# Optimization experiments

Measured on AMD Instinct MI355X. Metric: run time of the kernel, lower is better.

Reference implementation:

```python
import jax, jax.numpy as jnp
import numpy as np

N_NODES = 50000
N_EDGES = 800000
D_IN = 64
D_OUT = 64
D_HID = 64
EPS = 1e-5


def _init_params(key):
    ks = jax.random.split(key, 12)
    s = 0.05
    p = {}
    p["W_lin"] = jax.random.normal(ks[0], (D_IN, D_OUT), jnp.float32) * s
    p["W_src"] = jax.random.normal(ks[1], (D_IN, D_OUT), jnp.float32) * s
    p["W_dst"] = jax.random.normal(ks[2], (D_IN, D_OUT), jnp.float32) * s
    p["pos_w1"] = jax.random.normal(ks[3], (3, D_HID), jnp.float32) * s
    p["pos_b1"] = jnp.zeros((D_HID,), jnp.float32)
    p["pos_w2"] = jax.random.normal(ks[4], (D_HID, D_OUT), jnp.float32) * s
    p["pos_b2"] = jnp.zeros((D_OUT,), jnp.float32)
    p["attn_w1"] = jax.random.normal(ks[5], (D_OUT, D_HID), jnp.float32) * s
    p["attn_b1"] = jnp.zeros((D_HID,), jnp.float32)
    p["attn_w2"] = jax.random.normal(ks[6], (D_HID, D_OUT), jnp.float32) * s
    p["attn_b2"] = jnp.zeros((D_OUT,), jnp.float32)
    p["gamma"] = jnp.ones((D_OUT,), jnp.float32)
    p["beta"] = jnp.zeros((D_OUT,), jnp.float32)
    return p


def setup_inputs() -> dict:
    key = jax.random.key(0)
    k1, k2, k3, k4 = jax.random.split(key, 4)
    inp = {
        "x": jax.random.normal(k1, (N_NODES, D_IN), jnp.float32),
        "pos": jax.random.normal(k2, (N_NODES, 3), jnp.float32),
        "edge_index": jax.random.randint(k3, (2, N_EDGES), 0, N_NODES, jnp.int64),
    }
    inp.update(_init_params(k4))
    return inp


def _segment_softmax(alpha, seg, num_segments):
    # channel-wise softmax over edges sharing the same destination node
    m = jax.ops.segment_max(alpha, seg, num_segments=num_segments)  # [N, D]
    e = jnp.exp(alpha - m[seg])
    z = jax.ops.segment_sum(e, seg, num_segments=num_segments)  # [N, D]
    return e / (z[seg] + 1e-16)


def reference(x, pos, edge_index, W_lin, W_src, W_dst,
              pos_w1, pos_b1, pos_w2, pos_b2,
              attn_w1, attn_b1, attn_w2, attn_b2, gamma, beta):
    N = x.shape[0]
    # add self loops (PointTransformerConv default add_self_loops=True)
    loops = jnp.arange(N, dtype=edge_index.dtype)
    src = jnp.concatenate([edge_index[0], loops])  # j
    dst = jnp.concatenate([edge_index[1], loops])  # i (aggregation target)

    x_val = x @ W_lin          # [N, D] value projection
    a_src = x @ W_src          # alpha_j source term
    a_dst = x @ W_dst          # alpha_i destination term

    # per-edge positional encoding: pos_nn(pos_i - pos_j), two Linears, no activation
    rel = pos[dst] - pos[src]                         # [E, 3]
    delta = (rel @ pos_w1 + pos_b1) @ pos_w2 + pos_b2  # [E, D]

    # attention logits: attn_nn(alpha_i - alpha_j + delta)
    alpha = a_dst[dst] - a_src[src] + delta
    alpha = (alpha @ attn_w1 + attn_b1) @ attn_w2 + attn_b2  # [E, D]
    alpha = _segment_softmax(alpha, dst, N)

    # message and scatter-sum aggregation
    msg = alpha * (x_val[src] + delta)                # [E, D]
    out = jax.ops.segment_sum(msg, dst, num_segments=N)  # [N, D]

    out = jax.nn.elu(out)

    # BatchNorm over nodes (training-mode batch stats, biased var, eps=1e-5)
    mean = jnp.mean(out, axis=0)
    var = jnp.var(out, axis=0)
    out = (out - mean) * jax.lax.rsqrt(var + EPS) * gamma + beta
    return out
```

## Files before the change

kernel.cpp:

```cpp
#include <hip/hip_runtime.h>
#include <cmath>


__device__ __forceinline__ unsigned bf16r(float f) {
    unsigned u = __float_as_uint(f);
    return (u + 0x7fffu + ((u >> 16) & 1u)) >> 16;
}
__device__ __forceinline__ float bfhi(unsigned u) { return __uint_as_float(u & 0xffff0000u); }
__device__ __forceinline__ float bflo(unsigned u) { return __uint_as_float(u << 16); }

__device__ __forceinline__ void gemm_tile(const float (*xs)[68], const float (*Wl)[64],
                                          int tx, int ty, float acc[4][4])
{
    #pragma unroll
    for (int i = 0; i < 4; ++i)
        #pragma unroll
        for (int j = 0; j < 4; ++j) acc[i][j] = 0.f;
    for (int k = 0; k < 64; k += 4) {
        float4 b0 = *(const float4*)&Wl[k + 0][4 * tx];
        float4 b1 = *(const float4*)&Wl[k + 1][4 * tx];
        float4 b2 = *(const float4*)&Wl[k + 2][4 * tx];
        float4 b3 = *(const float4*)&Wl[k + 3][4 * tx];
        #pragma unroll
        for (int i = 0; i < 4; ++i) {
            float4 a = *(const float4*)&xs[4 * ty + i][k];
            acc[i][0] += a.x * b0.x + a.y * b1.x + a.z * b2.x + a.w * b3.x;
            acc[i][1] += a.x * b0.y + a.y * b1.y + a.z * b2.y + a.w * b3.y;
            acc[i][2] += a.x * b0.z + a.y * b1.z + a.z * b2.z + a.w * b3.z;
            acc[i][3] += a.x * b0.w + a.y * b1.w + a.z * b2.w + a.w * b3.w;
        }
    }
}

__global__ __launch_bounds__(256) void k_pre1(
    const float* __restrict__ attn_w1, const float* __restrict__ attn_w2,
    const float* __restrict__ pos_w1, const float* __restrict__ pos_b1,
    const float* __restrict__ pos_w2, const float* __restrict__ pos_b2,
    float* __restrict__ A2, float* __restrict__ M3, float* __restrict__ bc)
{
    int t = threadIdx.x;
    if (blockIdx.x == 0) {
        __shared__ __align__(16) float As[64][68];
        __shared__ __align__(16) float Bs[64][64];
        int lk = t & 63, lr = t >> 6;
        for (int i = 0; i < 16; ++i) {
            As[lr + 4 * i][lk] = attn_w1[(lr + 4 * i) * 64 + lk];
            Bs[lr + 4 * i][lk] = attn_w2[(lr + 4 * i) * 64 + lk];
        }
        __syncthreads();
        int tx = t & 15, ty = t >> 4;
        float acc[4][4];
        gemm_tile(As, Bs, tx, ty, acc);
        #pragma unroll
        for (int i = 0; i < 4; ++i)
            *(float4*)&A2[(4 * ty + i) * 64 + 4 * tx] =
                make_float4(acc[i][0], acc[i][1], acc[i][2], acc[i][3]);
    } else {
        int c = t & 63, q = t >> 6;
        if (q < 3) {
            float acc = 0.f;
            for (int h = 0; h < 64; ++h) acc += pos_w1[q * 64 + h] * pos_w2[h * 64 + c];
            M3[q * 64 + c] = acc;
        } else {
            float accb = 0.f;
            for (int h = 0; h < 64; ++h) accb += pos_b1[h] * pos_w2[h * 64 + c];
            bc[c] = accb + pos_b2[c];
        }
    }
}

__global__ __launch_bounds__(256) void k_pre2(
    const float* __restrict__ W_src, const float* __restrict__ A2,
    const float* __restrict__ M3,
    float* __restrict__ Wsrc2, float* __restrict__ M5)
{
    int t = threadIdx.x;
    if (blockIdx.x == 0) {
        __shared__ __align__(16) float As[64][68];
        __shared__ __align__(16) float Bs[64][64];
        int lk = t & 63, lr = t >> 6;
        for (int i = 0; i < 16; ++i) {
            As[lr + 4 * i][lk] = W_src[(lr + 4 * i) * 64 + lk];
            Bs[lr + 4 * i][lk] = A2[(lr + 4 * i) * 64 + lk];
        }
        __syncthreads();
        int tx = t & 15, ty = t >> 4;
        float acc[4][4];
        gemm_tile(As, Bs, tx, ty, acc);
        #pragma unroll
        for (int i = 0; i < 4; ++i)
            *(float4*)&Wsrc2[(4 * ty + i) * 64 + 4 * tx] =
                make_float4(acc[i][0], acc[i][1], acc[i][2], acc[i][3]);
    } else {
        int c = t & 63, q = t >> 6;
        if (q < 3) {
            float acc = 0.f;
            for (int k = 0; k < 64; ++k) acc += M3[q * 64 + k] * A2[k * 64 + c];
            M5[q * 64 + c] = acc;
        }
    }
}

__global__ __launch_bounds__(256, 4) void k_gemm_pair(
    const float* __restrict__ x, const float* __restrict__ pos,
    const float* __restrict__ Wsrc2, const float* __restrict__ Wlin,
    const float* __restrict__ M3, const float* __restrict__ M5,
    unsigned* __restrict__ pairbf, int n_nodes)
{
    __shared__ __align__(16) float xs[64][68];
    __shared__ __align__(16) float Wl[64][64];
    __shared__ float ps[192];
    __shared__ float m3s[192], m5s[192];
    int t = threadIdx.x;
    int tx = t & 15;
    int ty = t >> 4;
    int nbase = blockIdx.x * 64;
    int lk = t & 63;
    int lr = t >> 6;

    for (int i = 0; i < 16; ++i) {
        int n = lr + 4 * i;
        int gn = nbase + n;
        xs[n][lk] = (gn < n_nodes) ? x[gn * 64 + lk] : 0.f;
    }
    if (t < 192) {
        int gi = nbase * 3 + t;
        ps[t] = (gi < n_nodes * 3) ? pos[gi] : 0.f;
        m3s[t] = M3[t];
        m5s[t] = M5[t];
    }
    for (int i = 0; i < 16; ++i) Wl[lr + 4 * i][lk] = Wsrc2[(lr + 4 * i) * 64 + lk];
    __syncthreads();

    float acc_s[4][4];
    gemm_tile(xs, Wl, tx, ty, acc_s);

    __syncthreads();
    for (int i = 0; i < 16; ++i) Wl[lr + 4 * i][lk] = Wlin[(lr + 4 * i) * 64 + lk];
    __syncthreads();

    float acc_x[4][4];
    gemm_tile(xs, Wl, tx, ty, acc_x);

    #pragma unroll
    for (int i = 0; i < 4; ++i) {
        int n = 4 * ty + i;
        int gn = nbase + n;
        if (gn < n_nodes) {
            float px = ps[3 * n], py = ps[3 * n + 1], pz = ps[3 * n + 2];
            int c0 = 4 * tx;
            float g50 = px * m5s[c0]     + py * m5s[64 + c0]     + pz * m5s[128 + c0];
            float g51 = px * m5s[c0 + 1] + py * m5s[64 + c0 + 1] + pz * m5s[128 + c0 + 1];
            float g52 = px * m5s[c0 + 2] + py * m5s[64 + c0 + 2] + pz * m5s[128 + c0 + 2];
            float g53 = px * m5s[c0 + 3] + py * m5s[64 + c0 + 3] + pz * m5s[128 + c0 + 3];
            float g30 = px * m3s[c0]     + py * m3s[64 + c0]     + pz * m3s[128 + c0];
            float g31 = px * m3s[c0 + 1] + py * m3s[64 + c0 + 1] + pz * m3s[128 + c0 + 1];
            float g32 = px * m3s[c0 + 2] + py * m3s[64 + c0 + 2] + pz * m3s[128 + c0 + 2];
            float g33 = px * m3s[c0 + 3] + py * m3s[64 + c0 + 3] + pz * m3s[128 + c0 + 3];
            uint4 w;
            w.x = (bf16r(__expf(-(acc_s[i][0] + g50))) << 16) | bf16r(acc_x[i][0] - g30);
            w.y = (bf16r(__expf(-(acc_s[i][1] + g51))) << 16) | bf16r(acc_x[i][1] - g31);
            w.z = (bf16r(__expf(-(acc_s[i][2] + g52))) << 16) | bf16r(acc_x[i][2] - g32);
            w.w = (bf16r(__expf(-(acc_s[i][3] + g53))) << 16) | bf16r(acc_x[i][3] - g33);
            *(uint4*)&pairbf[gn * 64 + c0] = w;
        }
    }
}

__global__ __launch_bounds__(256) void k_hist(const int* __restrict__ ei,
                                              int* __restrict__ cnt, int n_edges)
{
    int i = blockIdx.x * blockDim.x + threadIdx.x;
    if (i < n_edges) atomicAdd(&cnt[ei[n_edges + i]], 1);
}

#define SCAN_CHUNK 4096

__global__ __launch_bounds__(256) void k_scan_partial(const int* __restrict__ cnt,
                                                      int* __restrict__ bsum, int n)
{
    __shared__ int wsh[4];
    int b = blockIdx.x, t = threadIdx.x;
    int base = b * SCAN_CHUNK + t * 16;
    int s = 0;
    #pragma unroll
    for (int i = 0; i < 16; ++i) {
        int idx = base + i;
        if (idx < n) s += cnt[idx];
    }
    for (int off = 32; off; off >>= 1) s += __shfl_down(s, off, 64);
    int lane = t & 63, wv = t >> 6;
    if (lane == 0) wsh[wv] = s;
    __syncthreads();
    if (t == 0) bsum[b] = wsh[0] + wsh[1] + wsh[2] + wsh[3];
}

__global__ void k_scan_base(const int* __restrict__ bsum, int* __restrict__ bbase,
                            int* __restrict__ rowptr, int nch, int n, int n_edges)
{
    if (threadIdx.x == 0) {
        int acc = 0;
        for (int c = 0; c < nch; ++c) { int tmp = bsum[c]; bbase[c] = acc; acc += tmp; }
        rowptr[n] = n_edges;
    }
}

__global__ __launch_bounds__(256) void k_scan_final(const int* __restrict__ cnt,
                                                    const int* __restrict__ bbase,
                                                    int* __restrict__ rowptr,
                                                    int* __restrict__ cursor, int n)
{
    __shared__ int wsh[4];
    int b = blockIdx.x, t = threadIdx.x;
    int base = b * SCAN_CHUNK + t * 16;
    int v[16];
    int s = 0;
    #pragma unroll
    for (int i = 0; i < 16; ++i) {
        int idx = base + i;
        v[i] = (idx < n) ? cnt[idx] : 0;
        s += v[i];
    }
    int lane = t & 63, wv = t >> 6;
    int inc = s;
    for (int off = 1; off < 64; off <<= 1) {
        int u = __shfl_up(inc, off, 64);
        if (lane >= off) inc += u;
    }
    if (lane == 63) wsh[wv] = inc;
    __syncthreads();
    if (t == 0) {
        int acc = 0;
        for (int w = 0; w < 4; ++w) { int tmp = wsh[w]; wsh[w] = acc; acc += tmp; }
    }
    __syncthreads();
    int run = bbase[b] + wsh[wv] + inc - s;
    #pragma unroll
    for (int i = 0; i < 16; ++i) {
        int idx = base + i;
        if (idx < n) {
            rowptr[idx] = run;
            cursor[idx] = run;
            run += v[i];
        }
    }
}

__global__ __launch_bounds__(256) void k_scatter(const int* __restrict__ ei,
                                                 int* __restrict__ cursor,
                                                 int* __restrict__ csr_src,
                                                 int n_edges)
{
    int i = blockIdx.x * blockDim.x + threadIdx.x;
    if (i < n_edges) {
        int dst = ei[n_edges + i];
        int p = atomicAdd(&cursor[dst], 1);
        csr_src[p] = ei[i] * 64;
    }
}

__global__ __launch_bounds__(256) void k_gather(
    const int* __restrict__ rowptr, const int* __restrict__ csr_src,
    const unsigned* __restrict__ pairbf, const float* __restrict__ pos,
    const float* __restrict__ M3, const float* __restrict__ bc,
    float* __restrict__ out, float* __restrict__ stats, int n_nodes)
{
    int t = threadIdx.x;
    int c = t & 63;
    float bcc = bc[c];
    float m30 = M3[c], m31 = M3[64 + c], m32 = M3[128 + c];

    int wid = (blockIdx.x * blockDim.x + t) >> 6;
    int nw = (gridDim.x * blockDim.x) >> 6;

    float lsum = 0.f, lsq = 0.f;

    for (int i = wid; i < n_nodes; i += nw) {
        int beg = rowptr[i], end = rowptr[i + 1];
        float px = pos[3 * i], py = pos[3 * i + 1], pz = pos[3 * i + 2];
        float ddi = bcc + px * m30 + py * m31 + pz * m32;
        unsigned up = pairbf[i * 64 + c];
        float w = bfhi(up);
        float zz = w;
        float SS = w * (bflo(up) + ddi);

        int k = beg;
        for (; k + 8 <= end; k += 8) {
            int s0 = csr_src[k],     s1 = csr_src[k + 1];
            int s2 = csr_src[k + 2], s3 = csr_src[k + 3];
            int s4 = csr_src[k + 4], s5 = csr_src[k + 5];
            int s6 = csr_src[k + 6], s7 = csr_src[k + 7];
            unsigned u0 = pairbf[s0 + c], u1 = pairbf[s1 + c];
            unsigned u2 = pairbf[s2 + c], u3 = pairbf[s3 + c];
            unsigned u4 = pairbf[s4 + c], u5 = pairbf[s5 + c];
            unsigned u6 = pairbf[s6 + c], u7 = pairbf[s7 + c];
            float w0 = bfhi(u0), w1 = bfhi(u1), w2 = bfhi(u2), w3 = bfhi(u3);
            float w4 = bfhi(u4), w5 = bfhi(u5), w6 = bfhi(u6), w7 = bfhi(u7);
            zz += ((w0 + w1) + (w2 + w3)) + ((w4 + w5) + (w6 + w7));
            SS += w0 * (bflo(u0) + ddi) + w1 * (bflo(u1) + ddi)
                + w2 * (bflo(u2) + ddi) + w3 * (bflo(u3) + ddi)
                + w4 * (bflo(u4) + ddi) + w5 * (bflo(u5) + ddi)
                + w6 * (bflo(u6) + ddi) + w7 * (bflo(u7) + ddi);
        }
        for (; k < end; ++k) {
            unsigned u0 = pairbf[csr_src[k] + c];
            float w0 = bfhi(u0);
            zz += w0;
            SS += w0 * (bflo(u0) + ddi);
        }

        float v = SS / (zz + 1e-16f);
        v = (v > 0.f) ? v : expm1f(v);
        out[i * 64 + c] = v;
        lsum += v;
        lsq += v * v;
    }

    __shared__ float sred[256], sred2[256];
    sred[t] = lsum;
    sred2[t] = lsq;
    __syncthreads();
    if (t < 64) {
        float s = sred[t] + sred[t + 64] + sred[t + 128] + sred[t + 192];
        float q = sred2[t] + sred2[t + 64] + sred2[t + 128] + sred2[t + 192];
        unsafeAtomicAdd(&stats[t], s);
        unsafeAtomicAdd(&stats[64 + t], q);
    }
}

__global__ __launch_bounds__(256) void k_bn(
    float4* __restrict__ out4, const float* __restrict__ stats,
    const float* __restrict__ gamma, const float* __restrict__ beta,
    int total4, float inv_n)
{
    __shared__ float ssc[64], ssh[64];
    int t = threadIdx.x;
    if (t < 64) {
        float mean = stats[t] * inv_n;
        float var = stats[64 + t] * inv_n - mean * mean;
        float scale = (1.0f / sqrtf(var + 1e-5f)) * gamma[t];
        ssc[t] = scale;
        ssh[t] = beta[t] - mean * scale;
    }
    __syncthreads();
    for (int idx = blockIdx.x * blockDim.x + t; idx < total4;
         idx += gridDim.x * blockDim.x) {
        float4 v = out4[idx];
        int c0 = (idx << 2) & 63;
        v.x = v.x * ssc[c0]     + ssh[c0];
        v.y = v.y * ssc[c0 + 1] + ssh[c0 + 1];
        v.z = v.z * ssc[c0 + 2] + ssh[c0 + 2];
        v.w = v.w * ssc[c0 + 3] + ssh[c0 + 3];
        out4[idx] = v;
    }
}

extern "C" void kernel_launch(void* const* d_in, const int* in_sizes, int n_in,
                              void* d_out, int out_size, void* d_ws, size_t ws_size,
                              hipStream_t stream)
{
    const float* x        = (const float*)d_in[0];
    const float* pos      = (const float*)d_in[1];
    const int*   ei       = (const int*)d_in[2];
    const float* W_lin    = (const float*)d_in[3];
    const float* W_src    = (const float*)d_in[4];
    const float* pos_w1   = (const float*)d_in[6];
    const float* pos_b1   = (const float*)d_in[7];
    const float* pos_w2   = (const float*)d_in[8];
    const float* pos_b2   = (const float*)d_in[9];
    const float* attn_w1  = (const float*)d_in[10];
    const float* attn_w2  = (const float*)d_in[12];
    const float* gamma    = (const float*)d_in[14];
    const float* beta     = (const float*)d_in[15];

    int n_nodes = in_sizes[0] / 64;
    int n_edges = in_sizes[2] / 2;
    int total = n_nodes * 64;
    int nch = (n_nodes + SCAN_CHUNK - 1) / SCAN_CHUNK;

    unsigned* pairbf = (unsigned*)d_ws;
    float* A2    = (float*)(pairbf + total);
    float* Wsrc2 = A2 + 4096;
    float* M3    = Wsrc2 + 4096;
    float* M5    = M3 + 192;
    float* bc    = M5 + 192;
    float* stats = bc + 64;
    int*   cnt     = (int*)(stats + 128);
    int*   rowptr  = cnt + n_nodes;
    int*   cursor  = rowptr + n_nodes + 1;
    int*   csr_src = cursor + n_nodes;
    int*   bsum    = csr_src + n_edges;
    int*   bbase   = bsum + 64;

    hipMemsetAsync(cnt, 0, (size_t)n_nodes * sizeof(int), stream);
    hipMemsetAsync(stats, 0, 128 * sizeof(float), stream);

    k_pre1<<<2, 256, 0, stream>>>(attn_w1, attn_w2, pos_w1, pos_b1, pos_w2,
                                  pos_b2, A2, M3, bc);
    k_pre2<<<2, 256, 0, stream>>>(W_src, A2, M3, Wsrc2, M5);
    k_gemm_pair<<<(n_nodes + 63) / 64, 256, 0, stream>>>(
        x, pos, Wsrc2, W_lin, M3, M5, pairbf, n_nodes);
    k_hist<<<(n_edges + 255) / 256, 256, 0, stream>>>(ei, cnt, n_edges);
    k_scan_partial<<<nch, 256, 0, stream>>>(cnt, bsum, n_nodes);
    k_scan_base<<<1, 64, 0, stream>>>(bsum, bbase, rowptr, nch, n_nodes, n_edges);
    k_scan_final<<<nch, 256, 0, stream>>>(cnt, bbase, rowptr, cursor, n_nodes);
    k_scatter<<<(n_edges + 255) / 256, 256, 0, stream>>>(ei, cursor, csr_src, n_edges);
    k_gather<<<2048, 256, 0, stream>>>(rowptr, csr_src, pairbf, pos, M3, bc,
                                       (float*)d_out, stats, n_nodes);
    k_bn<<<2048, 256, 0, stream>>>((float4*)d_out, stats, gamma, beta, total / 4,
                                   1.0f / (float)n_nodes);
}
```

Before: 223.0 us.

## Fuse memsets, histogram and scan-base into neighbouring kernels to cut launches

Zeroing of the count and stats buffers moves into extra blocks of the first precompute kernel, replacing two memsets. The edge histogram runs in extra blocks appended to the node GEMM kernel, so the two overlap inside one launch. The separate single-thread scan-base kernel is folded into the final scan, where each block sums the preceding block totals itself. The gather loop also factors the per-node positional term out of the weighted sum and adds it after normalisation, saving an add per edge but dropping the 1e-16 guard on the denominator.

```diff
diff --git a/kernel.cpp b/kernel.cpp
--- a/kernel.cpp
+++ b/kernel.cpp
@@ -36,7 +36,8 @@
     const float* __restrict__ attn_w1, const float* __restrict__ attn_w2,
     const float* __restrict__ pos_w1, const float* __restrict__ pos_b1,
     const float* __restrict__ pos_w2, const float* __restrict__ pos_b2,
-    float* __restrict__ A2, float* __restrict__ M3, float* __restrict__ bc)
+    float* __restrict__ A2, float* __restrict__ M3, float* __restrict__ bc,
+    int* __restrict__ cnt, float* __restrict__ stats, int n_nodes)
 {
     int t = threadIdx.x;
     if (blockIdx.x == 0) {
@@ -55,7 +56,7 @@
         for (int i = 0; i < 4; ++i)
             *(float4*)&A2[(4 * ty + i) * 64 + 4 * tx] =
                 make_float4(acc[i][0], acc[i][1], acc[i][2], acc[i][3]);
-    } else {
+    } else if (blockIdx.x == 1) {
         int c = t & 63, q = t >> 6;
         if (q < 3) {
             float acc = 0.f;
@@ -66,6 +67,11 @@
             for (int h = 0; h < 64; ++h) accb += pos_b1[h] * pos_w2[h * 64 + c];
             bc[c] = accb + pos_b2[c];
         }
+    } else {
+        if (blockIdx.x == 2 && t < 128) stats[t] = 0.f;
+        int idx = (blockIdx.x - 2) * 256 + t;
+        int stride = (gridDim.x - 2) * 256;
+        for (int i = idx; i < n_nodes; i += stride) cnt[i] = 0;
     }
 }
 
@@ -101,17 +107,25 @@
     }
 }
 
-__global__ __launch_bounds__(256, 4) void k_gemm_pair(
+__global__ __launch_bounds__(256, 4) void k_gemm_pair_hist(
     const float* __restrict__ x, const float* __restrict__ pos,
     const float* __restrict__ Wsrc2, const float* __restrict__ Wlin,
     const float* __restrict__ M3, const float* __restrict__ M5,
-    unsigned* __restrict__ pairbf, int n_nodes)
-{
+    unsigned* __restrict__ pairbf, int n_nodes,
+    const int* __restrict__ ei, int* __restrict__ cnt, int n_edges, int G)
+{
+    int t = threadIdx.x;
+    if ((int)blockIdx.x >= G) {
+        int idx = ((int)blockIdx.x - G) * 256 + t;
+        int stride = ((int)gridDim.x - G) * 256;
+        for (int i = idx; i < n_edges; i += stride)
+            atomicAdd(&cnt[ei[n_edges + i]], 1);
+        return;
+    }
     __shared__ __align__(16) float xs[64][68];
     __shared__ __align__(16) float Wl[64][64];
     __shared__ float ps[192];
     __shared__ float m3s[192], m5s[192];
-    int t = threadIdx.x;
     int tx = t & 15;
     int ty = t >> 4;
     int nbase = blockIdx.x * 64;
@@ -167,13 +181,6 @@
     }
 }
 
-__global__ __launch_bounds__(256) void k_hist(const int* __restrict__ ei,
-                                              int* __restrict__ cnt, int n_edges)
-{
-    int i = blockIdx.x * blockDim.x + threadIdx.x;
-    if (i < n_edges) atomicAdd(&cnt[ei[n_edges + i]], 1);
-}
-
 #define SCAN_CHUNK 4096
 
 __global__ __launch_bounds__(256) void k_scan_partial(const int* __restrict__ cnt,
@@ -195,23 +202,21 @@
     if (t == 0) bsum[b] = wsh[0] + wsh[1] + wsh[2] + wsh[3];
 }
 
-__global__ void k_scan_base(const int* __restrict__ bsum, int* __restrict__ bbase,
-                            int* __restrict__ rowptr, int nch, int n, int n_edges)
-{
-    if (threadIdx.x == 0) {
+__global__ __launch_bounds__(256) void k_scan_final(const int* __restrict__ cnt,
+                                                    const int* __restrict__ bsum,
+                                                    int* __restrict__ rowptr,
+                                                    int* __restrict__ cursor,
+                                                    int n, int nch, int n_edges)
+{
+    __shared__ int wsh[4];
+    __shared__ int bb;
+    int b = blockIdx.x, t = threadIdx.x;
+    if (t == 0) {
         int acc = 0;
-        for (int c = 0; c < nch; ++c) { int tmp = bsum[c]; bbase[c] = acc; acc += tmp; }
-        rowptr[n] = n_edges;
-    }
-}
-
-__global__ __launch_bounds__(256) void k_scan_final(const int* __restrict__ cnt,
-                                                    const int* __restrict__ bbase,
-                                                    int* __restrict__ rowptr,
-                                                    int* __restrict__ cursor, int n)
-{
-    __shared__ int wsh[4];
-    int b = blockIdx.x, t = threadIdx.x;
+        for (int c = 0; c < b; ++c) acc += bsum[c];
+        bb = acc;
+        if (b == nch - 1) rowptr[n] = n_edges;
+    }
     int base = b * SCAN_CHUNK + t * 16;
     int v[16];
     int s = 0;
@@ -234,7 +239,7 @@
         for (int w = 0; w < 4; ++w) { int tmp = wsh[w]; wsh[w] = acc; acc += tmp; }
     }
     __syncthreads();
-    int run = bbase[b] + wsh[wv] + inc - s;
+    int run = bb + wsh[wv] + inc - s;
     #pragma unroll
     for (int i = 0; i < 16; ++i) {
         int idx = base + i;
@@ -282,7 +287,7 @@
         unsigned up = pairbf[i * 64 + c];
         float w = bfhi(up);
         float zz = w;
-        float SS = w * (bflo(up) + ddi);
+        float SS = w * bflo(up);
 
         int k = beg;
         for (; k + 8 <= end; k += 8) {
@@ -297,19 +302,17 @@
             float w0 = bfhi(u0), w1 = bfhi(u1), w2 = bfhi(u2), w3 = bfhi(u3);
             float w4 = bfhi(u4), w5 = bfhi(u5), w6 = bfhi(u6), w7 = bfhi(u7);
             zz += ((w0 + w1) + (w2 + w3)) + ((w4 + w5) + (w6 + w7));
-            SS += w0 * (bflo(u0) + ddi) + w1 * (bflo(u1) + ddi)
-                + w2 * (bflo(u2) + ddi) + w3 * (bflo(u3) + ddi)
-                + w4 * (bflo(u4) + ddi) + w5 * (bflo(u5) + ddi)
-                + w6 * (bflo(u6) + ddi) + w7 * (bflo(u7) + ddi);
+            SS += w0 * bflo(u0) + w1 * bflo(u1) + w2 * bflo(u2) + w3 * bflo(u3)
+                + w4 * bflo(u4) + w5 * bflo(u5) + w6 * bflo(u6) + w7 * bflo(u7);
         }
         for (; k < end; ++k) {
             unsigned u0 = pairbf[csr_src[k] + c];
             float w0 = bfhi(u0);
             zz += w0;
-            SS += w0 * (bflo(u0) + ddi);
-        }
-
-        float v = SS / (zz + 1e-16f);
+            SS += w0 * bflo(u0);
+        }
+
+        float v = SS / zz + ddi;
         v = (v > 0.f) ? v : expm1f(v);
         out[i * 64 + c] = v;
         lsum += v;
@@ -390,20 +393,17 @@
     int*   cursor  = rowptr + n_nodes + 1;
     int*   csr_src = cursor + n_nodes;
     int*   bsum    = csr_src + n_edges;
-    int*   bbase   = bsum + 64;
-
-    hipMemsetAsync(cnt, 0, (size_t)n_nodes * sizeof(int), stream);
-    hipMemsetAsync(stats, 0, 128 * sizeof(float), stream);
-
-    k_pre1<<<2, 256, 0, stream>>>(attn_w1, attn_w2, pos_w1, pos_b1, pos_w2,
-                                  pos_b2, A2, M3, bc);
+
+    int G = (n_nodes + 63) / 64;
+
+    k_pre1<<<18, 256, 0, stream>>>(attn_w1, attn_w2, pos_w1, pos_b1, pos_w2,
+                                   pos_b2, A2, M3, bc, cnt, stats, n_nodes);
     k_pre2<<<2, 256, 0, stream>>>(W_src, A2, M3, Wsrc2, M5);
-    k_gemm_pair<<<(n_nodes + 63) / 64, 256, 0, stream>>>(
-        x, pos, Wsrc2, W_lin, M3, M5, pairbf, n_nodes);
-    k_hist<<<(n_edges + 255) / 256, 256, 0, stream>>>(ei, cnt, n_edges);
+    k_gemm_pair_hist<<<G + 512, 256, 0, stream>>>(
+        x, pos, Wsrc2, W_lin, M3, M5, pairbf, n_nodes, ei, cnt, n_edges, G);
     k_scan_partial<<<nch, 256, 0, stream>>>(cnt, bsum, n_nodes);
-    k_scan_base<<<1, 64, 0, stream>>>(bsum, bbase, rowptr, nch, n_nodes, n_edges);
-    k_scan_final<<<nch, 256, 0, stream>>>(cnt, bbase, rowptr, cursor, n_nodes);
+    k_scan_final<<<nch, 256, 0, stream>>>(cnt, bsum, rowptr, cursor,
+                                          n_nodes, nch, n_edges);
     k_scatter<<<(n_edges + 255) / 256, 256, 0, stream>>>(ei, cursor, csr_src, n_edges);
     k_gather<<<2048, 256, 0, stream>>>(rowptr, csr_src, pairbf, pos, M3, bc,
                                        (float*)d_out, stats, n_nodes);
```

New measurement: 203.6 us. -8.7%, faster.
